# Performance work log

Measured on AMD Instinct MI355X. Metric: run time of the kernel, lower is better.

The kernel has to match this reference:

```python
import jax, jax.numpy as jnp
import numpy as np

B, L, D, H = 2, 2048, 1024, 16
DK = D // H


def setup_inputs() -> dict:
    key = jax.random.key(0)
    ks = jax.random.split(key, 11)
    s = 0.02
    return {
        "q": jax.random.normal(ks[0], (B, L, D), jnp.float32),
        "k": jax.random.normal(ks[1], (B, L, D), jnp.float32),
        "v": jax.random.normal(ks[2], (B, L, D), jnp.float32),
        "mask": jnp.ones((B, 1, 1, L), jnp.int32),
        "wq": jax.random.normal(ks[3], (D, D), jnp.float32) * s,
        "bq": jnp.zeros((D,), jnp.float32),
        "wk": jax.random.normal(ks[4], (D, D), jnp.float32) * s,
        "bk": jnp.zeros((D,), jnp.float32),
        "wv": jax.random.normal(ks[5], (D, D), jnp.float32) * s,
        "bv": jnp.zeros((D,), jnp.float32),
        "wo": jax.random.normal(ks[6], (D, D), jnp.float32) * s,
        "bo": jnp.zeros((D,), jnp.float32),
    }


def _split_heads(x):
    # (B, L, D) -> (B, H, L, DK)
    return x.reshape(B, L, H, DK).transpose(0, 2, 1, 3)


def reference(q, k, v, mask, wq, bq, wk, bk, wv, bv, wo, bo):
    query = _split_heads(q @ wq.T + bq)
    key = _split_heads(k @ wk.T + bk)
    value = _split_heads(v @ wv.T + bv)
    scale = 1.0 / jnp.sqrt(jnp.asarray(DK, query.dtype))
    # (B, H, Lq, Lk) materialized scores, as in the original module
    scores = jnp.einsum('bhqd,bhkd->bhqk', query, key) * scale
    scores = jnp.where(mask == 0, jnp.asarray(-1e9, scores.dtype), scores)
    weights = jax.nn.softmax(scores, axis=-1)
    out = jnp.einsum('bhqk,bhkd->bhqd', weights, value)
    out = out.transpose(0, 2, 1, 3).reshape(B, L, D)
    return out @ wo.T + bo
```

## Files before the change

### kernel.cpp

```cpp
#include <hip/hip_runtime.h>
#include <hip/hip_bf16.h>


#define DEVINL __device__ __forceinline__

typedef __attribute__((ext_vector_type(8))) short short8;
typedef __attribute__((ext_vector_type(4))) float floatx4;

static constexpr int Bq = 2, Lq = 2048, Dm = 1024;
static constexpr int Mrows = Bq * Lq;
static constexpr size_t QKV_LD = 3072;
static constexpr int NT = Lq / 64;

DEVINL unsigned short f2bf(float x) {
  __hip_bfloat16 h = __float2bfloat16(x);
  unsigned short u;
  __builtin_memcpy(&u, &h, 2);
  return u;
}

DEVINL float bf2f(unsigned short u) {
  unsigned int t = ((unsigned int)u) << 16;
  float f;
  __builtin_memcpy(&f, &t, 4);
  return f;
}

DEVINL short8 cvt8(float4 a, float4 b) {
  union { unsigned short u[8]; short8 v; } o;
  o.u[0] = f2bf(a.x); o.u[1] = f2bf(a.y); o.u[2] = f2bf(a.z); o.u[3] = f2bf(a.w);
  o.u[4] = f2bf(b.x); o.u[5] = f2bf(b.y); o.u[6] = f2bf(b.z); o.u[7] = f2bf(b.w);
  return o.v;
}

DEVINL void gll16(const void* g, const void* l) {
  auto gp = (const __attribute__((address_space(1))) char*)(unsigned long long)(uintptr_t)g;
  auto lp = (__attribute__((address_space(3))) char*)(unsigned int)(uintptr_t)l;
  __builtin_amdgcn_global_load_lds(gp, lp, 16, 0, 0);
}

template <bool A_BF16, bool OUT_BF16>
__global__ __launch_bounds__(256) void gemm_k(
    const void* __restrict__ A0, const void* __restrict__ A1, const void* __restrict__ A2,
    const float* __restrict__ W0, const float* __restrict__ W1, const float* __restrict__ W2,
    const float* __restrict__ b0, const float* __restrict__ b1, const float* __restrict__ b2,
    void* __restrict__ Cout, int M, int N, int K, int ldc) {
  const int z = blockIdx.z;
  const void* Aany = (z == 0) ? A0 : ((z == 1) ? A1 : A2);
  const float* W = (z == 0) ? W0 : ((z == 1) ? W1 : W2);
  const float* bias = (z == 0) ? b0 : ((z == 1) ? b1 : b2);
  const int m0 = blockIdx.x * 128, n0 = blockIdx.y * 128;
  const int tid = threadIdx.x, lane = tid & 63, w = tid >> 6;
  const int wr = w >> 1, wc = w & 1;

  __shared__ __align__(16) unsigned short As[2][128 * 32];
  __shared__ __align__(16) unsigned short Bs[2][128 * 32];

  floatx4 acc[4][4] = {};
  float4 wreg[2][2], areg[2][2];

  auto loadW = [&](int kt) {
#pragma unroll
    for (int it = 0; it < 2; ++it) {
      int g = it * 256 + tid, row = g >> 2, gk = g & 3;
      const float* p = W + (size_t)(n0 + row) * K + kt + gk * 8;
      wreg[it][0] = ((const float4*)p)[0];
      wreg[it][1] = ((const float4*)p)[1];
    }
  };
  auto loadA = [&](int kt) {
#pragma unroll
    for (int it = 0; it < 2; ++it) {
      int g = it * 256 + tid, row = g >> 2, gk = g & 3;
      const float* p = (const float*)Aany + (size_t)(m0 + row) * K + kt + gk * 8;
      areg[it][0] = ((const float4*)p)[0];
      areg[it][1] = ((const float4*)p)[1];
    }
  };
  auto writeW = [&](int buf) {
#pragma unroll
    for (int it = 0; it < 2; ++it) {
      int g = it * 256 + tid, row = g >> 2, gk = g & 3;
      *(short8*)((char*)Bs + buf * 8192 + row * 64 + ((gk ^ (row & 3)) << 4)) =
          cvt8(wreg[it][0], wreg[it][1]);
    }
  };
  auto writeA = [&](int buf) {
#pragma unroll
    for (int it = 0; it < 2; ++it) {
      int g = it * 256 + tid, row = g >> 2, gk = g & 3;
      *(short8*)((char*)As + buf * 8192 + row * 64 + ((gk ^ (row & 3)) << 4)) =
          cvt8(areg[it][0], areg[it][1]);
    }
  };
  auto stageA = [&](int kt, int buf) {
#pragma unroll
    for (int it = 0; it < 2; ++it) {
      int g = it * 256 + tid, row = g >> 2, gk = g & 3;
      int koff = (gk ^ (row & 3)) * 8;
      gll16((const unsigned short*)Aany + (size_t)(m0 + row) * K + kt + koff,
            (const char*)As + buf * 8192 + (it * 256 + w * 64) * 16);
    }
  };

  const int nt = K / 32;
  loadW(0);
  if (!A_BF16) loadA(0);
  writeW(0);
  if (A_BF16) stageA(0, 0); else writeA(0);
  if (nt > 1) { loadW(32); if (!A_BF16) loadA(32); }
  __syncthreads();

  const int krow = lane >> 4;
  for (int t = 0; t < nt; ++t) {
    const int c = t & 1, n = c ^ 1;
    short8 af[4], bfr[4];
#pragma unroll
    for (int m = 0; m < 4; ++m) {
      int row = wr * 64 + m * 16 + (lane & 15);
      af[m] = *(const short8*)((const char*)As + c * 8192 + row * 64 + ((krow ^ (row & 3)) << 4));
    }
#pragma unroll
    for (int n2 = 0; n2 < 4; ++n2) {
      int row = wc * 64 + n2 * 16 + (lane & 15);
      bfr[n2] = *(const short8*)((const char*)Bs + c * 8192 + row * 64 + ((krow ^ (row & 3)) << 4));
    }
    __builtin_amdgcn_s_setprio(1);
#pragma unroll
    for (int m = 0; m < 4; ++m)
#pragma unroll
      for (int n2 = 0; n2 < 4; ++n2)
        acc[m][n2] = __builtin_amdgcn_mfma_f32_16x16x32_bf16(af[m], bfr[n2], acc[m][n2], 0, 0, 0);
    __builtin_amdgcn_s_setprio(0);
    if (t + 1 < nt) {
      writeW(n);
      if (A_BF16) stageA((t + 1) * 32, n); else writeA(n);
      if (t + 2 < nt) { loadW((t + 2) * 32); if (!A_BF16) loadA((t + 2) * 32); }
    }
    __syncthreads();
  }

  const int r4 = lane >> 4;
#pragma unroll
  for (int m = 0; m < 4; ++m)
#pragma unroll
    for (int n2 = 0; n2 < 4; ++n2) {
      int col = n0 + wc * 64 + n2 * 16 + (lane & 15);
      float bv = bias[col];
#pragma unroll
      for (int r = 0; r < 4; ++r) {
        int row = m0 + wr * 64 + m * 16 + r4 * 4 + r;
        float v = acc[m][n2][r] + bv;
        if (OUT_BF16)
          ((unsigned short*)Cout)[(size_t)row * ldc + (size_t)z * N + col] = f2bf(v);
        else
          ((float*)Cout)[(size_t)row * ldc + (size_t)z * N + col] = v;
      }
    }
}

__global__ __launch_bounds__(256) void attn_kernel(const unsigned short* __restrict__ QKV,
                                                   const int* __restrict__ mask,
                                                   unsigned short* __restrict__ Aout) {
  const int bh = blockIdx.y, b = bh >> 4, h = bh & 15;
  const int q0 = blockIdx.x * 64;
  const int tid = threadIdx.x, lane = tid & 63, w = tid >> 6;

  __shared__ __align__(16) unsigned short Klds[2][64 * 64];
  __shared__ __align__(16) unsigned short Vtlds[2][64 * 64];
  __shared__ __align__(16) unsigned short Plds[4][16 * 64];
  __shared__ int mflag[NT];

  const unsigned short* base = QKV + (size_t)b * Lq * QKV_LD;
  const unsigned short* Kbase = base + 1024;
  const unsigned short* Vbase = base + 2048;

  const int kp = tid & 31;
  const int vd0 = (tid >> 5) * 8;

  auto stageK = [&](int t, int buf) {
#pragma unroll
    for (int it = 0; it < 2; ++it) {
      int g = it * 256 + tid, key = g >> 3, gk = g & 7;
      gll16(Kbase + (size_t)(t * 64 + key) * QKV_LD + h * 64 + (gk ^ (key & 7)) * 8,
            (const char*)Klds + buf * 8192 + (it * 256 + w * 64) * 16);
    }
  };
  short8 vr0, vr1;
  auto loadV = [&](int t) {
    vr0 = *(const short8*)(Vbase + (size_t)(t * 64 + 2 * kp) * QKV_LD + h * 64 + vd0);
    vr1 = *(const short8*)(Vbase + (size_t)(t * 64 + 2 * kp + 1) * QKV_LD + h * 64 + vd0);
  };
  auto writeV = [&](int buf) {
#pragma unroll
    for (int i = 0; i < 8; ++i) {
      int d = vd0 + i;
      unsigned int val = (unsigned int)(unsigned short)vr0[i] |
                         ((unsigned int)(unsigned short)vr1[i] << 16);
      *(unsigned int*)((char*)Vtlds + buf * 8192 + d * 128 + (((kp >> 2) ^ (d & 7)) << 4) +
                       (kp & 3) * 4) = val;
    }
  };

  stageK(0, 0);
  loadV(0);
  writeV(0);
  {
    const int* mp = mask + b * Lq + tid * 8;
    int4 a = ((const int4*)mp)[0], bb = ((const int4*)mp)[1];
    int myall = (a.x && a.y && a.z && a.w && bb.x && bb.y && bb.z && bb.w) ? 1 : 0;
    unsigned long long bal = __ballot(myall);
    if (lane < 8) mflag[w * 8 + lane] = (((bal >> (lane * 8)) & 0xffull) == 0xffull);
  }

  short8 qf[2];
  {
    int row = q0 + w * 16 + (lane & 15);
#pragma unroll
    for (int c = 0; c < 2; ++c) {
      short8 raw = *(const short8*)(base + (size_t)row * QKV_LD + h * 64 + c * 32 + (lane >> 4) * 8);
      union { unsigned short u[8]; short8 v; } o2;
#pragma unroll
      for (int i = 0; i < 8; ++i) o2.u[i] = f2bf(bf2f((unsigned short)raw[i]) * 0.125f);
      qf[c] = o2.v;
    }
  }
  union { unsigned short u[8]; short8 v; } one_u;
#pragma unroll
  for (int i = 0; i < 8; ++i) one_u.u[i] = 0x3F80;
  const short8 ones8 = one_u.v;

  __syncthreads();

  floatx4 o[4] = {};
  floatx4 lacc = {};
  float mrow[4];
#pragma unroll
  for (int r = 0; r < 4; ++r) mrow[r] = -1e30f;

  for (int t = 0; t < NT; ++t) {
    const int c = t & 1, n = c ^ 1;
    if (t + 1 < NT) { stageK(t + 1, n); loadV(t + 1); }

    floatx4 s[4] = {};
    __builtin_amdgcn_s_setprio(1);
#pragma unroll
    for (int f = 0; f < 4; ++f) {
      int key = f * 16 + (lane & 15);
#pragma unroll
      for (int c2 = 0; c2 < 2; ++c2) {
        short8 kf = *(const short8*)((const char*)Klds + c * 8192 + key * 128 +
                                     (((c2 * 4 + (lane >> 4)) ^ (key & 7)) << 4));
        s[f] = __builtin_amdgcn_mfma_f32_16x16x32_bf16(qf[c2], kf, s[f], 0, 0, 0);
      }
    }
    __builtin_amdgcn_s_setprio(0);

    float tmax[4];
#pragma unroll
    for (int r = 0; r < 4; ++r)
      tmax[r] = fmaxf(fmaxf(s[0][r], s[1][r]), fmaxf(s[2][r], s[3][r]));
    const int allm = mflag[t];
    bool ok = (tmax[0] <= mrow[0] + 8.f) && (tmax[1] <= mrow[1] + 8.f) &&
              (tmax[2] <= mrow[2] + 8.f) && (tmax[3] <= mrow[3] + 8.f);
    if (__ballot(ok && allm) == ~0ull) {
#pragma unroll
      for (int f = 0; f < 4; ++f)
#pragma unroll
        for (int r = 0; r < 4; ++r) s[f][r] = __expf(s[f][r] - mrow[r]);
    } else {
#pragma unroll
      for (int dx = 1; dx <= 8; dx <<= 1)
#pragma unroll
        for (int r = 0; r < 4; ++r) tmax[r] = fmaxf(tmax[r], __shfl_xor(tmax[r], dx, 64));
      float mnew[4], alpha[4];
#pragma unroll
      for (int r = 0; r < 4; ++r) {
        mnew[r] = fmaxf(mrow[r], tmax[r]);
        alpha[r] = __expf(mrow[r] - mnew[r]);
        mrow[r] = mnew[r];
      }
#pragma unroll
      for (int df = 0; df < 4; ++df)
#pragma unroll
        for (int r = 0; r < 4; ++r) o[df][r] *= alpha[r];
#pragma unroll
      for (int r = 0; r < 4; ++r) lacc[r] *= alpha[r];
      if (allm) {
#pragma unroll
        for (int f = 0; f < 4; ++f)
#pragma unroll
          for (int r = 0; r < 4; ++r) s[f][r] = __expf(s[f][r] - mnew[r]);
      } else {
#pragma unroll
        for (int f = 0; f < 4; ++f) {
          int mv = mask[b * Lq + t * 64 + f * 16 + (lane & 15)];
#pragma unroll
          for (int r = 0; r < 4; ++r)
            s[f][r] = mv ? __expf(s[f][r] - mnew[r]) : 0.f;
        }
      }
    }

#pragma unroll
    for (int f = 0; f < 4; ++f)
#pragma unroll
      for (int r = 0; r < 4; ++r) {
        int row = (lane >> 4) * 4 + r, col = f * 16 + (lane & 15);
        *(unsigned short*)((char*)&Plds[w][0] + row * 128 + (((col >> 3) ^ (row & 7)) << 4) +
                           (col & 7) * 2) = f2bf(s[f][r]);
      }

    short8 pf[2];
#pragma unroll
    for (int kc = 0; kc < 2; ++kc)
      pf[kc] = *(const short8*)((const char*)&Plds[w][0] + (lane & 15) * 128 +
                                (((kc * 4 + (lane >> 4)) ^ (lane & 7)) << 4));
    __builtin_amdgcn_s_setprio(1);
    lacc = __builtin_amdgcn_mfma_f32_16x16x32_bf16(pf[0], ones8, lacc, 0, 0, 0);
    lacc = __builtin_amdgcn_mfma_f32_16x16x32_bf16(pf[1], ones8, lacc, 0, 0, 0);
#pragma unroll
    for (int df = 0; df < 4; ++df) {
      int d = df * 16 + (lane & 15);
#pragma unroll
      for (int kc = 0; kc < 2; ++kc) {
        short8 vf = *(const short8*)((const char*)Vtlds + c * 8192 + d * 128 +
                                     (((kc * 4 + (lane >> 4)) ^ (d & 7)) << 4));
        o[df] = __builtin_amdgcn_mfma_f32_16x16x32_bf16(pf[kc], vf, o[df], 0, 0, 0);
      }
    }
    __builtin_amdgcn_s_setprio(0);

    if (t + 1 < NT) writeV(n);
    __syncthreads();
  }

  float rl[4];
#pragma unroll
  for (int r = 0; r < 4; ++r) rl[r] = 1.0f / lacc[r];
#pragma unroll
  for (int df = 0; df < 4; ++df)
#pragma unroll
    for (int r = 0; r < 4; ++r) {
      int row = q0 + w * 16 + (lane >> 4) * 4 + r;
      int col = h * 64 + df * 16 + (lane & 15);
      Aout[(size_t)(b * Lq + row) * Dm + col] = f2bf(o[df][r] * rl[r]);
    }
}

extern "C" void kernel_launch(void* const* d_in, const int* in_sizes, int n_in,
                              void* d_out, int out_size, void* d_ws, size_t ws_size,
                              hipStream_t stream) {
  const float* q = (const float*)d_in[0];
  const float* k = (const float*)d_in[1];
  const float* v = (const float*)d_in[2];
  const int* maskp = (const int*)d_in[3];
  const float* wq = (const float*)d_in[4];
  const float* bq = (const float*)d_in[5];
  const float* wk = (const float*)d_in[6];
  const float* bk = (const float*)d_in[7];
  const float* wv = (const float*)d_in[8];
  const float* bv = (const float*)d_in[9];
  const float* wo = (const float*)d_in[10];
  const float* bo = (const float*)d_in[11];

  unsigned short* qkv = (unsigned short*)d_ws;
  unsigned short* attnout = qkv + (size_t)Mrows * QKV_LD;

  gemm_k<false, true><<<dim3(Mrows / 128, Dm / 128, 3), 256, 0, stream>>>(
      q, k, v, wq, wk, wv, bq, bk, bv, qkv, Mrows, Dm, Dm, (int)QKV_LD);

  attn_kernel<<<dim3(Lq / 64, Bq * 16), 256, 0, stream>>>(qkv, maskp, attnout);

  gemm_k<true, false><<<dim3(Mrows / 128, Dm / 128, 1), 256, 0, stream>>>(
      attnout, attnout, attnout, wo, wo, wo, bo, bo, bo, d_out, Mrows, Dm, Dm, Dm);
}
```

Measured before the change: 276.3 us.

## Remap blocks to XCDs, use exp2 softmax, reorder GEMM prefetch before MFMA

Both GEMM and attention kernels now use a 1D grid with an XCD-aware remap, so blocks that share A rows or the same head land on the same XCD and get better L2 reuse. Attention folds log2(e) into the Q scale and uses the hardware exp2 instead of __expf, with the rescale threshold scaled to match. The GEMM loop now issues the next-tile LDS writes and global loads before the MFMA block rather than after it, to overlap memory with compute. The remap hardcodes the grid shapes, so it depends on the fixed problem sizes.

```diff
diff --git a/kernel.cpp b/kernel.cpp
--- a/kernel.cpp
+++ b/kernel.cpp
@@ -45,11 +45,15 @@
     const float* __restrict__ W0, const float* __restrict__ W1, const float* __restrict__ W2,
     const float* __restrict__ b0, const float* __restrict__ b1, const float* __restrict__ b2,
     void* __restrict__ Cout, int M, int N, int K, int ldc) {
-  const int z = blockIdx.z;
+  const int bid = blockIdx.x;
+  const int xcd = bid & 7, sl = bid >> 3;
+  const int g = xcd + ((sl >> 3) << 3), jn = sl & 7;
+  const int z = g >> 5;
+  const int m0 = (g & 31) * 128, n0 = jn * 128;
+
   const void* Aany = (z == 0) ? A0 : ((z == 1) ? A1 : A2);
   const float* W = (z == 0) ? W0 : ((z == 1) ? W1 : W2);
   const float* bias = (z == 0) ? b0 : ((z == 1) ? b1 : b2);
-  const int m0 = blockIdx.x * 128, n0 = blockIdx.y * 128;
   const int tid = threadIdx.x, lane = tid & 63, w = tid >> 6;
   const int wr = w >> 1, wc = w & 1;
 
@@ -62,7 +66,7 @@
   auto loadW = [&](int kt) {
 #pragma unroll
     for (int it = 0; it < 2; ++it) {
-      int g = it * 256 + tid, row = g >> 2, gk = g & 3;
+      int gg = it * 256 + tid, row = gg >> 2, gk = gg & 3;
       const float* p = W + (size_t)(n0 + row) * K + kt + gk * 8;
       wreg[it][0] = ((const float4*)p)[0];
       wreg[it][1] = ((const float4*)p)[1];
@@ -71,7 +75,7 @@
   auto loadA = [&](int kt) {
 #pragma unroll
     for (int it = 0; it < 2; ++it) {
-      int g = it * 256 + tid, row = g >> 2, gk = g & 3;
+      int gg = it * 256 + tid, row = gg >> 2, gk = gg & 3;
       const float* p = (const float*)Aany + (size_t)(m0 + row) * K + kt + gk * 8;
       areg[it][0] = ((const float4*)p)[0];
       areg[it][1] = ((const float4*)p)[1];
@@ -80,7 +84,7 @@
   auto writeW = [&](int buf) {
 #pragma unroll
     for (int it = 0; it < 2; ++it) {
-      int g = it * 256 + tid, row = g >> 2, gk = g & 3;
+      int gg = it * 256 + tid, row = gg >> 2, gk = gg & 3;
       *(short8*)((char*)Bs + buf * 8192 + row * 64 + ((gk ^ (row & 3)) << 4)) =
           cvt8(wreg[it][0], wreg[it][1]);
     }
@@ -88,7 +92,7 @@
   auto writeA = [&](int buf) {
 #pragma unroll
     for (int it = 0; it < 2; ++it) {
-      int g = it * 256 + tid, row = g >> 2, gk = g & 3;
+      int gg = it * 256 + tid, row = gg >> 2, gk = gg & 3;
       *(short8*)((char*)As + buf * 8192 + row * 64 + ((gk ^ (row & 3)) << 4)) =
           cvt8(areg[it][0], areg[it][1]);
     }
@@ -96,7 +100,7 @@
   auto stageA = [&](int kt, int buf) {
 #pragma unroll
     for (int it = 0; it < 2; ++it) {
-      int g = it * 256 + tid, row = g >> 2, gk = g & 3;
+      int gg = it * 256 + tid, row = gg >> 2, gk = gg & 3;
       int koff = (gk ^ (row & 3)) * 8;
       gll16((const unsigned short*)Aany + (size_t)(m0 + row) * K + kt + koff,
             (const char*)As + buf * 8192 + (it * 256 + w * 64) * 16);
@@ -125,18 +129,18 @@
       int row = wc * 64 + n2 * 16 + (lane & 15);
       bfr[n2] = *(const short8*)((const char*)Bs + c * 8192 + row * 64 + ((krow ^ (row & 3)) << 4));
     }
-    __builtin_amdgcn_s_setprio(1);
-#pragma unroll
-    for (int m = 0; m < 4; ++m)
-#pragma unroll
-      for (int n2 = 0; n2 < 4; ++n2)
-        acc[m][n2] = __builtin_amdgcn_mfma_f32_16x16x32_bf16(af[m], bfr[n2], acc[m][n2], 0, 0, 0);
-    __builtin_amdgcn_s_setprio(0);
     if (t + 1 < nt) {
       writeW(n);
       if (A_BF16) stageA((t + 1) * 32, n); else writeA(n);
       if (t + 2 < nt) { loadW((t + 2) * 32); if (!A_BF16) loadA((t + 2) * 32); }
     }
+    __builtin_amdgcn_s_setprio(1);
+#pragma unroll
+    for (int m = 0; m < 4; ++m)
+#pragma unroll
+      for (int n2 = 0; n2 < 4; ++n2)
+        acc[m][n2] = __builtin_amdgcn_mfma_f32_16x16x32_bf16(af[m], bfr[n2], acc[m][n2], 0, 0, 0);
+    __builtin_amdgcn_s_setprio(0);
     __syncthreads();
   }
 
@@ -162,8 +166,11 @@
 __global__ __launch_bounds__(256) void attn_kernel(const unsigned short* __restrict__ QKV,
                                                    const int* __restrict__ mask,
                                                    unsigned short* __restrict__ Aout) {
-  const int bh = blockIdx.y, b = bh >> 4, h = bh & 15;
-  const int q0 = blockIdx.x * 64;
+  const int bid = blockIdx.x;
+  const int xcd = bid & 7, sl = bid >> 3;
+  const int bh = xcd + ((sl >> 5) << 3);
+  const int q0 = (sl & 31) * 64;
+  const int b = bh >> 4, h = bh & 15;
   const int tid = threadIdx.x, lane = tid & 63, w = tid >> 6;
 
   __shared__ __align__(16) unsigned short Klds[2][64 * 64];
@@ -221,7 +228,7 @@
       short8 raw = *(const short8*)(base + (size_t)row * QKV_LD + h * 64 + c * 32 + (lane >> 4) * 8);
       union { unsigned short u[8]; short8 v; } o2;
 #pragma unroll
-      for (int i = 0; i < 8; ++i) o2.u[i] = f2bf(bf2f((unsigned short)raw[i]) * 0.125f);
+      for (int i = 0; i < 8; ++i) o2.u[i] = f2bf(bf2f((unsigned short)raw[i]) * 0.18033688f);
       qf[c] = o2.v;
     }
   }
@@ -261,13 +268,13 @@
     for (int r = 0; r < 4; ++r)
       tmax[r] = fmaxf(fmaxf(s[0][r], s[1][r]), fmaxf(s[2][r], s[3][r]));
     const int allm = mflag[t];
-    bool ok = (tmax[0] <= mrow[0] + 8.f) && (tmax[1] <= mrow[1] + 8.f) &&
-              (tmax[2] <= mrow[2] + 8.f) && (tmax[3] <= mrow[3] + 8.f);
+    bool ok = (tmax[0] <= mrow[0] + 11.5f) && (tmax[1] <= mrow[1] + 11.5f) &&
+              (tmax[2] <= mrow[2] + 11.5f) && (tmax[3] <= mrow[3] + 11.5f);
     if (__ballot(ok && allm) == ~0ull) {
 #pragma unroll
       for (int f = 0; f < 4; ++f)
 #pragma unroll
-        for (int r = 0; r < 4; ++r) s[f][r] = __expf(s[f][r] - mrow[r]);
+        for (int r = 0; r < 4; ++r) s[f][r] = __builtin_amdgcn_exp2f(s[f][r] - mrow[r]);
     } else {
 #pragma unroll
       for (int dx = 1; dx <= 8; dx <<= 1)
@@ -277,7 +284,7 @@
 #pragma unroll
       for (int r = 0; r < 4; ++r) {
         mnew[r] = fmaxf(mrow[r], tmax[r]);
-        alpha[r] = __expf(mrow[r] - mnew[r]);
+        alpha[r] = __builtin_amdgcn_exp2f(mrow[r] - mnew[r]);
         mrow[r] = mnew[r];
       }
 #pragma unroll
@@ -290,14 +297,14 @@
 #pragma unroll
         for (int f = 0; f < 4; ++f)
 #pragma unroll
-          for (int r = 0; r < 4; ++r) s[f][r] = __expf(s[f][r] - mnew[r]);
+          for (int r = 0; r < 4; ++r) s[f][r] = __builtin_amdgcn_exp2f(s[f][r] - mnew[r]);
       } else {
 #pragma unroll
         for (int f = 0; f < 4; ++f) {
           int mv = mask[b * Lq + t * 64 + f * 16 + (lane & 15)];
 #pragma unroll
           for (int r = 0; r < 4; ++r)
-            s[f][r] = mv ? __expf(s[f][r] - mnew[r]) : 0.f;
+            s[f][r] = mv ? __builtin_amdgcn_exp2f(s[f][r] - mnew[r]) : 0.f;
         }
       }
     }
@@ -367,11 +374,11 @@
   unsigned short* qkv = (unsigned short*)d_ws;
   unsigned short* attnout = qkv + (size_t)Mrows * QKV_LD;
 
-  gemm_k<false, true><<<dim3(Mrows / 128, Dm / 128, 3), 256, 0, stream>>>(
+  gemm_k<false, true><<<dim3(768), 256, 0, stream>>>(
       q, k, v, wq, wk, wv, bq, bk, bv, qkv, Mrows, Dm, Dm, (int)QKV_LD);
 
-  attn_kernel<<<dim3(Lq / 64, Bq * 16), 256, 0, stream>>>(qkv, maskp, attnout);
-
-  gemm_k<true, false><<<dim3(Mrows / 128, Dm / 128, 1), 256, 0, stream>>>(
+  attn_kernel<<<dim3(1024), 256, 0, stream>>>(qkv, maskp, attnout);
+
+  gemm_k<true, false><<<dim3(256), 256, 0, stream>>>(
       attnout, attnout, attnout, wo, wo, wo, bo, bo, bo, d_out, Mrows, Dm, Dm, Dm);
 }
```

After: 278.3 us. Within noise of the previous version (+0.7%).
